# Performance work log

Hardware: AMD Instinct MI355X
Metric: run time of the kernel (lower is better)

Reference implementation:

```python
import jax, jax.numpy as jnp
import numpy as np

N_VOX = 200_000
C = 64
B, G = 2, 128  # batch size, grid resolution per axis
K = 27         # 3x3x3 kernel volume
EPS = 1e-5


def _build_coords_and_kernel_map(seed=0):
    """Build unique voxel coords on a [B,G,G,G] grid and the 27-offset kernel map.

    nbr[i, k] = row index of the voxel at coord[i] + offset[k], or N_VOX if absent
    (sentinel row that gathers zeros). This mirrors MinkowskiEngine's
    coordinate-hash in/out kernel maps for a stride-1 conv.
    """
    rng = np.random.default_rng(seed)
    total = B * G * G * G
    keys = np.sort(rng.choice(total, size=N_VOX, replace=False).astype(np.int64))
    z = keys % G
    y = (keys // G) % G
    x = (keys // (G * G)) % G
    b = keys // (G * G * G)
    offs = [(dx, dy, dz) for dx in (-1, 0, 1) for dy in (-1, 0, 1) for dz in (-1, 0, 1)]
    nbr = np.full((N_VOX, K), N_VOX, dtype=np.int64)
    for k, (dx, dy, dz) in enumerate(offs):
        nx, ny, nz = x + dx, y + dy, z + dz
        valid = (nx >= 0) & (nx < G) & (ny >= 0) & (ny < G) & (nz >= 0) & (nz < G)
        nkey = ((b * G + nx) * G + ny) * G + nz
        pos = np.clip(np.searchsorted(keys, nkey), 0, N_VOX - 1)
        found = valid & (keys[pos] == nkey)
        nbr[:, k] = np.where(found, pos, N_VOX)
    return jnp.asarray(nbr)


def setup_inputs() -> dict:
    key = jax.random.key(0)
    ks = jax.random.split(key, 12)
    w_scale = 1.0 / np.sqrt(K * C)
    inp = {
        "feats": jax.random.normal(ks[0], (N_VOX, C), jnp.float32),
        "nbr": _build_coords_and_kernel_map(),
        "W1": jax.random.normal(ks[1], (K, C, C), jnp.float32) * w_scale,
        "g1": 1.0 + 0.1 * jax.random.normal(ks[2], (C,), jnp.float32),
        "b1": 0.1 * jax.random.normal(ks[3], (C,), jnp.float32),
        "m1": 0.1 * jax.random.normal(ks[4], (C,), jnp.float32),
        "v1": jax.random.uniform(ks[5], (C,), jnp.float32, 0.5, 1.5),
        "W2": jax.random.normal(ks[6], (K, C, C), jnp.float32) * w_scale,
        "g2": 1.0 + 0.1 * jax.random.normal(ks[7], (C,), jnp.float32),
        "b2": 0.1 * jax.random.normal(ks[8], (C,), jnp.float32),
        "m2": 0.1 * jax.random.normal(ks[9], (C,), jnp.float32),
        "v2": jax.random.uniform(ks[10], (C,), jnp.float32, 0.5, 1.5),
    }
    return inp


def _bn(x, g, b, m, v):
    # MinkowskiBatchNorm, eval mode: per-channel affine with running stats
    return (x - m) * (g * jax.lax.rsqrt(v + EPS)) + b


def _sparse_conv(feats, nbr, W):
    # gather-GEMM-scatter sparse 3D conv over the precomputed kernel map.
    # Sentinel index N_VOX gathers the appended zero row (missing neighbor).
    fpad = jnp.concatenate([feats, jnp.zeros((1, feats.shape[1]), feats.dtype)], axis=0)
    out = jnp.zeros((feats.shape[0], W.shape[2]), feats.dtype)
    for k in range(W.shape[0]):  # fixed 27-tap loop (structural, not data dim)
        out = out + fpad[nbr[:, k]] @ W[k]
    return out


def reference(feats, nbr, W1, g1, b1, m1, v1, W2, g2, b2, m2, v2):
    h = jax.nn.relu(_bn(_sparse_conv(feats, nbr, W1), g1, b1, m1, v1))
    h = _bn(_sparse_conv(h, nbr, W2), g2, b2, m2, v2)
    # in_channels == out_channels and stride == 1 -> identity shortcut
    return jax.nn.relu(h + feats)
```

## Files before the change

### kernel.cpp

```cpp
#include <hip/hip_runtime.h>
#include <hip/hip_bf16.h>

#define NVOX 200000
#define NTAP 27
#define OSTR 68
#define ROWB 128

typedef __bf16          bf16x8 __attribute__((ext_vector_type(8)));
typedef unsigned short  u16x8  __attribute__((ext_vector_type(8)));
typedef float           f32x4  __attribute__((ext_vector_type(4)));

#define FB_BYTES    ((size_t)(NVOX + 1) * ROWB)
#define WSHUF_BYTES (NTAP * 2 * 4 * 64 * 16)
#define FB_OFF      0
#define H_OFF       (FB_BYTES)
#define WS1_OFF     (2 * FB_BYTES)
#define WS2_OFF     (WS1_OFF + WSHUF_BYTES)
#define FLAG_OFF    (WS2_OFF + WSHUF_BYTES)

static __device__ __forceinline__ unsigned short f2bf_bits(float f) {
    __hip_bfloat16 h = __float2bfloat16(f);
    union { __hip_bfloat16 h; unsigned short u; } u; u.h = h; return u.u;
}
static __device__ __forceinline__ float bf2f(unsigned short s) {
    union { float f; unsigned u; } u; u.u = ((unsigned)s) << 16; return u.f;
}
static __device__ __forceinline__ float ld_param(const void* p, int c, int isbf) {
    return isbf ? bf2f(((const unsigned short*)p)[c]) : ((const float*)p)[c];
}
static __device__ __forceinline__ void gload_lds16(const void* gp, void* lp) {
    __builtin_amdgcn_global_load_lds(
        (const __attribute__((address_space(1))) void*)gp,
        (__attribute__((address_space(3))) void*)lp, 16, 0, 0);
}
static __device__ __forceinline__ int wave_isbf(const unsigned* v1w) {
    int l = threadIdx.x & 63;
    int ok = 1;
    if (l < 32) {
        unsigned w = v1w[l], lo = w & 0xFFFFu, hi = w >> 16;
        ok = (lo >= 0x3F00u && lo <= 0x3FC0u && hi >= 0x3F00u && hi <= 0x3FC0u);
    }
    return __all(ok);
}

__global__ __launch_bounds__(256)
void prep_kernel(const void* __restrict__ feats,
                 const void* __restrict__ W1, const void* __restrict__ W2,
                 const unsigned* __restrict__ v1w, const unsigned* __restrict__ nbrw,
                 uint4* __restrict__ fbuf, uint4* __restrict__ hbuf,
                 uint4* __restrict__ Ws1, uint4* __restrict__ Ws2,
                 int* __restrict__ flags) {
    const int bx = blockIdx.x;
    if (bx < 6250) {
        const int isbf = wave_isbf(v1w);
        size_t t = (size_t)bx * 256 + threadIdx.x;
        if (isbf) {
            fbuf[t] = ((const uint4*)feats)[t];
        } else {
            float4 a = ((const float4*)feats)[2 * t];
            float4 b = ((const float4*)feats)[2 * t + 1];
            union { uint4 q; unsigned short u[8]; } o;
            o.u[0] = f2bf_bits(a.x); o.u[1] = f2bf_bits(a.y);
            o.u[2] = f2bf_bits(a.z); o.u[3] = f2bf_bits(a.w);
            o.u[4] = f2bf_bits(b.x); o.u[5] = f2bf_bits(b.y);
            o.u[6] = f2bf_bits(b.z); o.u[7] = f2bf_bits(b.w);
            fbuf[t] = o.q;
        }
    } else if (bx < 6358) {
        const int isbf = wave_isbf(v1w);
        int t = (bx - 6250) * 256 + threadIdx.x;
        const void* W = (t < 13824) ? W1 : W2;
        uint4* Ws     = (t < 13824) ? Ws1 : Ws2;
        int f = (t < 13824) ? t : t - 13824;
        int k  = f / 512;
        int r  = f % 512;
        int kc = r / 256;
        int r2 = r % 256;
        int nc = r2 / 64;
        int l  = r2 % 64;
        int quad = l >> 4, li = l & 15;
        unsigned short tmp[8];
#pragma unroll
        for (int j = 0; j < 8; ++j) {
            int off = k * 4096 + (kc * 32 + quad * 8 + j) * 64 + (nc * 16 + li);
            tmp[j] = isbf ? ((const unsigned short*)W)[off]
                          : f2bf_bits(((const float*)W)[off]);
        }
        uint4 v;
        v.x = (unsigned)tmp[0] | ((unsigned)tmp[1] << 16);
        v.y = (unsigned)tmp[2] | ((unsigned)tmp[3] << 16);
        v.z = (unsigned)tmp[4] | ((unsigned)tmp[5] << 16);
        v.w = (unsigned)tmp[6] | ((unsigned)tmp[7] << 16);
        Ws[f] = v;
    } else {
        int t = threadIdx.x;
        if (t < 64) {
            int isbf = wave_isbf(v1w);
            int n64ok = 1;
#pragma unroll
            for (int i = 0; i < 8; ++i)
                if (nbrw[2 * (t * 8 + i) + 1] != 0u) n64ok = 0;
            int n64 = __all(n64ok);
            if (t == 0) { flags[0] = isbf; flags[1] = n64; }
        }
        uint4 z = make_uint4(0u, 0u, 0u, 0u);
        if (t >= 64 && t < 72) fbuf[(size_t)NVOX * 8 + (t - 64)] = z;
        if (t >= 72 && t < 80) hbuf[(size_t)NVOX * 8 + (t - 72)] = z;
    }
}

#define STG(kk, bp) do {                                                    \
    if ((mgw >> (kk)) & 1) {                                                \
        int ia_ = nbrLDS[r0 * NTAP + (kk)];                                 \
        int ib_ = nbrLDS[r1 * NTAP + (kk)];                                 \
        gload_lds16(srcB + (size_t)ia_ * ROWB + f0 * 16,                    \
                    (void*)((bp) + w * 128));                               \
        gload_lds16(srcB + (size_t)ib_ * ROWB + f1 * 16,                    \
                    (void*)((bp) + w * 128 + 64));                         \
    } } while (0)

#define LOADB(kk, B0, B1) do {                                              \
    B0 = Ws[(kk) * 512 + w * 64 + l];                                       \
    B1 = Ws[(kk) * 512 + 256 + w * 64 + l];                                 \
} while (0)

#define COMPUTE(kk, bp, B0, B1) do {                                        \
    _Pragma("unroll")                                                       \
    for (int g = 0; g < 4; ++g) {                                           \
        if ((mg[g] >> (kk)) & 1) {                                          \
            bf16x8 a0_ = *(const bf16x8*)((bp) + ro0[g]);                   \
            bf16x8 a1_ = *(const bf16x8*)((bp) + ro1[g]);                   \
            acc[g] = __builtin_amdgcn_mfma_f32_16x16x32_bf16(a0_, B0, acc[g], 0, 0, 0); \
            acc[g] = __builtin_amdgcn_mfma_f32_16x16x32_bf16(a1_, B1, acc[g], 0, 0, 0); \
        }                                                                   \
    }                                                                       \
} while (0)

__global__ __launch_bounds__(256, 7)
void conv_bn_kernel(const uint4* __restrict__ srcV,
                    const void* __restrict__ nbr,
                    const bf16x8* __restrict__ Ws,
                    const void* __restrict__ gg, const void* __restrict__ bb,
                    const void* __restrict__ mm, const void* __restrict__ vv,
                    const u16x8* __restrict__ resid,
                    const int* __restrict__ flags,
                    void* __restrict__ dst, int final_out) {
    __shared__ __align__(16) int smi[5828];
    int*   nbrLDS = smi;
    uint4* at0    = (uint4*)(smi + 1728);
    uint4* at1    = at0 + 512;
    int*   maskLDS = smi + 5824;
    float* outLDS = (float*)smi;

    const int tid  = threadIdx.x;
    const int base = blockIdx.x * 64;
    const int isbf = flags[0];
    const int n64  = flags[1];
    const char* srcB = (const char*)srcV;

    if (tid < 4) maskLDS[tid] = 0;
    __syncthreads();
    {
        if (!n64) {
            const int* np = (const int*)nbr + (long)base * NTAP;
            for (int i = tid; i < 64 * NTAP; i += 256) nbrLDS[i] = np[i];
        } else {
            const long long* np = (const long long*)nbr + (long)base * NTAP;
            for (int i = tid; i < 64 * NTAP; i += 256) nbrLDS[i] = (int)np[i];
        }
    }
    __syncthreads();

    if (tid < NTAP * 4) {
        int k = tid >> 2, g = tid & 3;
        int mn = 0x7fffffff;
#pragma unroll
        for (int r = 0; r < 16; ++r) mn = min(mn, nbrLDS[(g * 16 + r) * NTAP + k]);
        if (mn < NVOX) atomicOr(&maskLDS[g], 1 << k);
    }
    __syncthreads();

    const int w = tid >> 6, l = tid & 63;
    const int quad = l >> 4, li = l & 15;

    int mg[4];
#pragma unroll
    for (int g = 0; g < 4; ++g) mg[g] = __builtin_amdgcn_readfirstlane(maskLDS[g]);
    const int mgw = __builtin_amdgcn_readfirstlane(maskLDS[w]);

    const int s0 = w * 128 + l;
    const int s1 = s0 + 64;
    const int r0 = s0 >> 3, f0 = (s0 - r0) & 7;
    const int r1 = s1 >> 3, f1 = (s1 - r1) & 7;
    int ro0[4], ro1[4];
#pragma unroll
    for (int g = 0; g < 4; ++g) {
        int row = g * 16 + li;
        ro0[g] = row * 8 + ((quad + row) & 7);
        ro1[g] = row * 8 + ((quad + 4 + row) & 7);
    }

    f32x4 acc[4];
#pragma unroll
    for (int g = 0; g < 4; ++g) acc[g] = (f32x4){0.f, 0.f, 0.f, 0.f};

    bf16x8 xB0, xB1, yB0, yB1;

    STG(0, at0);
    LOADB(0, xB0, xB1);
    __syncthreads();

    for (int k = 0; k < 26; k += 2) {
        STG(k + 1, at1);
        LOADB(k + 1, yB0, yB1);
        COMPUTE(k, at0, xB0, xB1);
        __syncthreads();
        STG(k + 2, at0);
        LOADB(k + 2, xB0, xB1);
        COMPUTE(k + 1, at1, yB0, yB1);
        __syncthreads();
    }
    COMPUTE(26, at0, xB0, xB1);

    const int c = w * 16 + li;
    float scale = ld_param(gg, c, isbf) * rsqrtf(ld_param(vv, c, isbf) + 1e-5f);
    float offs  = ld_param(bb, c, isbf) - ld_param(mm, c, isbf) * scale;

    __syncthreads();
#pragma unroll
    for (int g = 0; g < 4; ++g)
#pragma unroll
        for (int r = 0; r < 4; ++r)
            outLDS[(g * 16 + quad * 4 + r) * OSTR + c] = acc[g][r] * scale + offs;
    __syncthreads();

    {
        int trow = tid >> 2, cc = tid & 3;
        long grow = base + trow;
        const float4* lp = (const float4*)&outLDS[trow * OSTR + cc * 16];
        float4 q0 = lp[0], q1 = lp[1], q2 = lp[2], q3 = lp[3];
        float vals[16] = {q0.x, q0.y, q0.z, q0.w, q1.x, q1.y, q1.z, q1.w,
                          q2.x, q2.y, q2.z, q2.w, q3.x, q3.y, q3.z, q3.w};

        if (resid) {
            const u16x8* rp = resid + grow * 8 + cc * 2;
            u16x8 r0v = rp[0], r1v = rp[1];
#pragma unroll
            for (int j = 0; j < 8; ++j) { vals[j] += bf2f(r0v[j]); vals[8 + j] += bf2f(r1v[j]); }
        }
#pragma unroll
        for (int j = 0; j < 16; ++j) vals[j] = fmaxf(vals[j], 0.f);

        const int store_bf = (!final_out) || isbf;
        if (store_bf) {
            u16x8 o0, o1;
#pragma unroll
            for (int j = 0; j < 8; ++j) { o0[j] = f2bf_bits(vals[j]); o1[j] = f2bf_bits(vals[8 + j]); }
            u16x8* dp = (u16x8*)dst + grow * 8 + cc * 2;
            dp[0] = o0; dp[1] = o1;
        } else {
            float4* dp = (float4*)dst + grow * 16 + cc * 4;
            dp[0] = (float4){vals[0], vals[1], vals[2], vals[3]};
            dp[1] = (float4){vals[4], vals[5], vals[6], vals[7]};
            dp[2] = (float4){vals[8], vals[9], vals[10], vals[11]};
            dp[3] = (float4){vals[12], vals[13], vals[14], vals[15]};
        }
    }
}

extern "C" void kernel_launch(void* const* d_in, const int* in_sizes, int n_in,
                              void* d_out, int out_size, void* d_ws, size_t ws_size,
                              hipStream_t stream) {
    const void* feats = d_in[0];
    const void* nbr   = d_in[1];
    const void* W1    = d_in[2];
    const void* g1    = d_in[3];
    const void* b1    = d_in[4];
    const void* m1    = d_in[5];
    const void* v1    = d_in[6];
    const void* W2    = d_in[7];
    const void* g2    = d_in[8];
    const void* b2    = d_in[9];
    const void* m2    = d_in[10];
    const void* v2    = d_in[11];

    char* ws = (char*)d_ws;
    uint4* fbuf = (uint4*)(ws + FB_OFF);
    uint4* hbuf = (uint4*)(ws + H_OFF);
    uint4* Ws1  = (uint4*)(ws + WS1_OFF);
    uint4* Ws2  = (uint4*)(ws + WS2_OFF);
    int*   flags = (int*)(ws + FLAG_OFF);

    prep_kernel<<<dim3(6359), dim3(256), 0, stream>>>(
        feats, W1, W2, (const unsigned*)v1, (const unsigned*)nbr,
        fbuf, hbuf, Ws1, Ws2, flags);

    conv_bn_kernel<<<dim3(NVOX / 64), dim3(256), 0, stream>>>(
        fbuf, nbr, (const bf16x8*)Ws1, g1, b1, m1, v1,
        nullptr, flags, hbuf, 0);

    conv_bn_kernel<<<dim3(NVOX / 64), dim3(256), 0, stream>>>(
        hbuf, nbr, (const bf16x8*)Ws2, g2, b2, m2, v2,
        (const u16x8*)fbuf, flags, d_out, 1);
}
```

Baseline: 242.7 us.

## Stage two taps per pipeline step and remap blocks across XCDs

The gather/MFMA loop now stages two kernel taps per buffer, so each __syncthreads covers two taps, which halves the number of barriers and deepens the prefetch. Block indices are remapped so that consecutive voxel tiles land on the same XCD, which should improve L2 locality for neighbour gathers. Launch bounds drop from 7 to 4 waves per SIMD to make room for the larger LDS footprint and the extra B registers. The cost is lower occupancy and therefore less latency hiding.

```diff
diff --git a/kernel.cpp b/kernel.cpp
--- a/kernel.cpp
+++ b/kernel.cpp
@@ -119,9 +119,9 @@
                     (void*)((bp) + w * 128 + 64));                         \
     } } while (0)
 
-#define LOADB(kk, B0, B1) do {                                              \
-    B0 = Ws[(kk) * 512 + w * 64 + l];                                       \
-    B1 = Ws[(kk) * 512 + 256 + w * 64 + l];                                 \
+#define LOADB(kk, B0r, B1r) do {                                            \
+    B0r = Ws[(kk) * 512 + w * 64 + l];                                      \
+    B1r = Ws[(kk) * 512 + 256 + w * 64 + l];                                \
 } while (0)
 
 #define COMPUTE(kk, bp, B0, B1) do {                                        \
@@ -136,7 +136,7 @@
     }                                                                       \
 } while (0)
 
-__global__ __launch_bounds__(256, 7)
+__global__ __launch_bounds__(256, 4)
 void conv_bn_kernel(const uint4* __restrict__ srcV,
                     const void* __restrict__ nbr,
                     const bf16x8* __restrict__ Ws,
@@ -145,15 +145,23 @@
                     const u16x8* __restrict__ resid,
                     const int* __restrict__ flags,
                     void* __restrict__ dst, int final_out) {
-    __shared__ __align__(16) int smi[5828];
-    int*   nbrLDS = smi;
-    uint4* at0    = (uint4*)(smi + 1728);
-    uint4* at1    = at0 + 512;
-    int*   maskLDS = smi + 5824;
-    float* outLDS = (float*)smi;
+    __shared__ __align__(16) int smi[1732 + 4 * 2048];
+    int*   nbrLDS  = smi;
+    int*   maskLDS = smi + 1728;
+    uint4* at0     = (uint4*)(smi + 1732);
+    uint4* at0b    = at0 + 512;
+    uint4* at1     = at0 + 1024;
+    uint4* at1b    = at0 + 1536;
+    float* outLDS  = (float*)smi;
 
     const int tid  = threadIdx.x;
-    const int base = blockIdx.x * 64;
+    const int nwg  = gridDim.x;
+    const int orig = blockIdx.x;
+    const int qq   = nwg >> 3, rr = nwg & 7;
+    const int xcd  = orig & 7, idx = orig >> 3;
+    const int bid  = (xcd < rr ? xcd * (qq + 1) : rr * (qq + 1) + (xcd - rr) * qq) + idx;
+    const int base = bid * 64;
+
     const int isbf = flags[0];
     const int n64  = flags[1];
     const char* srcB = (const char*)srcV;
@@ -204,23 +212,30 @@
 #pragma unroll
     for (int g = 0; g < 4; ++g) acc[g] = (f32x4){0.f, 0.f, 0.f, 0.f};
 
-    bf16x8 xB0, xB1, yB0, yB1;
-
-    STG(0, at0);
-    LOADB(0, xB0, xB1);
-    __syncthreads();
-
-    for (int k = 0; k < 26; k += 2) {
-        STG(k + 1, at1);
-        LOADB(k + 1, yB0, yB1);
-        COMPUTE(k, at0, xB0, xB1);
+    bf16x8 xB0, xB1, xB2, xB3, yB0, yB1, yB2, yB3;
+
+    STG(0, at0); STG(1, at0b);
+    LOADB(0, xB0, xB1); LOADB(1, xB2, xB3);
+    __syncthreads();
+
+    for (int k = 0; k < 24; k += 4) {
+        STG(k + 2, at1); STG(k + 3, at1b);
+        LOADB(k + 2, yB0, yB1); LOADB(k + 3, yB2, yB3);
+        COMPUTE(k,     at0,  xB0, xB1);
+        COMPUTE(k + 1, at0b, xB2, xB3);
         __syncthreads();
-        STG(k + 2, at0);
-        LOADB(k + 2, xB0, xB1);
-        COMPUTE(k + 1, at1, yB0, yB1);
+        STG(k + 4, at0); STG(k + 5, at0b);
+        LOADB(k + 4, xB0, xB1); LOADB(k + 5, xB2, xB3);
+        COMPUTE(k + 2, at1,  yB0, yB1);
+        COMPUTE(k + 3, at1b, yB2, yB3);
         __syncthreads();
     }
-    COMPUTE(26, at0, xB0, xB1);
+    STG(26, at1);
+    LOADB(26, yB0, yB1);
+    COMPUTE(24, at0,  xB0, xB1);
+    COMPUTE(25, at0b, xB2, xB3);
+    __syncthreads();
+    COMPUTE(26, at1, yB0, yB1);
 
     const int c = w * 16 + li;
     float scale = ld_param(gg, c, isbf) * rsqrtf(ld_param(vv, c, isbf) + 1e-5f);
```

Result: slower. 272.3 us (+12.2%).

## Shrink conv tiles to 32 voxels with 2-wave blocks and XCD-aware block remap

Applied to the files above, without the earlier changes.

Each conv block now handles 32 voxels with 128 threads instead of 64 voxels with 256 threads. Each wave computes two 16-channel output groups, so it holds four weight fragments per tap and issues four MFMAs per row group. Block indices are remapped so consecutive voxel chunks land on the same XCD, which should improve L2 locality of neighbor gathers. The smaller tiles give more blocks, less LDS per block and finer tap masks. In exchange, weight fragments are reloaded twice as often per voxel and each wave needs more registers.

```diff
diff --git a/kernel.cpp b/kernel.cpp
--- a/kernel.cpp
+++ b/kernel.cpp
@@ -5,6 +5,7 @@
 #define NTAP 27
 #define OSTR 68
 #define ROWB 128
+#define VPB  32
 
 typedef __bf16          bf16x8 __attribute__((ext_vector_type(8)));
 typedef unsigned short  u16x8  __attribute__((ext_vector_type(8)));
@@ -119,24 +120,28 @@
                     (void*)((bp) + w * 128 + 64));                         \
     } } while (0)
 
-#define LOADB(kk, B0, B1) do {                                              \
-    B0 = Ws[(kk) * 512 + w * 64 + l];                                       \
-    B1 = Ws[(kk) * 512 + 256 + w * 64 + l];                                 \
+#define LOADB4(kk, B00r, B01r, B10r, B11r) do {                             \
+    B00r = Ws[(kk) * 512 +       (2 * w) * 64 + l];                         \
+    B01r = Ws[(kk) * 512 + 256 + (2 * w) * 64 + l];                         \
+    B10r = Ws[(kk) * 512 +       (2 * w + 1) * 64 + l];                     \
+    B11r = Ws[(kk) * 512 + 256 + (2 * w + 1) * 64 + l];                     \
 } while (0)
 
-#define COMPUTE(kk, bp, B0, B1) do {                                        \
+#define COMPUTE(kk, bp, B00, B01, B10, B11) do {                            \
     _Pragma("unroll")                                                       \
-    for (int g = 0; g < 4; ++g) {                                           \
+    for (int g = 0; g < 2; ++g) {                                           \
         if ((mg[g] >> (kk)) & 1) {                                          \
             bf16x8 a0_ = *(const bf16x8*)((bp) + ro0[g]);                   \
             bf16x8 a1_ = *(const bf16x8*)((bp) + ro1[g]);                   \
-            acc[g] = __builtin_amdgcn_mfma_f32_16x16x32_bf16(a0_, B0, acc[g], 0, 0, 0); \
-            acc[g] = __builtin_amdgcn_mfma_f32_16x16x32_bf16(a1_, B1, acc[g], 0, 0, 0); \
+            acc[2*g+0] = __builtin_amdgcn_mfma_f32_16x16x32_bf16(a0_, B00, acc[2*g+0], 0, 0, 0); \
+            acc[2*g+0] = __builtin_amdgcn_mfma_f32_16x16x32_bf16(a1_, B01, acc[2*g+0], 0, 0, 0); \
+            acc[2*g+1] = __builtin_amdgcn_mfma_f32_16x16x32_bf16(a0_, B10, acc[2*g+1], 0, 0, 0); \
+            acc[2*g+1] = __builtin_amdgcn_mfma_f32_16x16x32_bf16(a1_, B11, acc[2*g+1], 0, 0, 0); \
         }                                                                   \
     }                                                                       \
 } while (0)
 
-__global__ __launch_bounds__(256, 7)
+__global__ __launch_bounds__(128, 6)
 void conv_bn_kernel(const uint4* __restrict__ srcV,
                     const void* __restrict__ nbr,
                     const bf16x8* __restrict__ Ws,
@@ -145,34 +150,40 @@
                     const u16x8* __restrict__ resid,
                     const int* __restrict__ flags,
                     void* __restrict__ dst, int final_out) {
-    __shared__ __align__(16) int smi[5828];
-    int*   nbrLDS = smi;
-    uint4* at0    = (uint4*)(smi + 1728);
-    uint4* at1    = at0 + 512;
-    int*   maskLDS = smi + 5824;
-    float* outLDS = (float*)smi;
+    __shared__ __align__(16) int smi[868 + 2 * 1024];
+    int*   nbrLDS  = smi;
+    int*   maskLDS = smi + 864;
+    uint4* at0     = (uint4*)(smi + 868);
+    uint4* at1     = at0 + 256;
+    float* outLDS  = (float*)smi;
 
     const int tid  = threadIdx.x;
-    const int base = blockIdx.x * 64;
+    const int nwg  = gridDim.x;
+    const int orig = blockIdx.x;
+    const int qq   = nwg >> 3, rr = nwg & 7;
+    const int xcd  = orig & 7, idx = orig >> 3;
+    const int bid  = (xcd < rr ? xcd * (qq + 1) : rr * (qq + 1) + (xcd - rr) * qq) + idx;
+    const int base = bid * VPB;
+
     const int isbf = flags[0];
     const int n64  = flags[1];
     const char* srcB = (const char*)srcV;
 
-    if (tid < 4) maskLDS[tid] = 0;
+    if (tid < 2) maskLDS[tid] = 0;
     __syncthreads();
     {
         if (!n64) {
             const int* np = (const int*)nbr + (long)base * NTAP;
-            for (int i = tid; i < 64 * NTAP; i += 256) nbrLDS[i] = np[i];
+            for (int i = tid; i < VPB * NTAP; i += 128) nbrLDS[i] = np[i];
         } else {
             const long long* np = (const long long*)nbr + (long)base * NTAP;
-            for (int i = tid; i < 64 * NTAP; i += 256) nbrLDS[i] = (int)np[i];
-        }
-    }
-    __syncthreads();
-
-    if (tid < NTAP * 4) {
-        int k = tid >> 2, g = tid & 3;
+            for (int i = tid; i < VPB * NTAP; i += 128) nbrLDS[i] = (int)np[i];
+        }
+    }
+    __syncthreads();
+
+    if (tid < NTAP * 2) {
+        int k = tid >> 1, g = tid & 1;
         int mn = 0x7fffffff;
 #pragma unroll
         for (int r = 0; r < 16; ++r) mn = min(mn, nbrLDS[(g * 16 + r) * NTAP + k]);
@@ -183,18 +194,18 @@
     const int w = tid >> 6, l = tid & 63;
     const int quad = l >> 4, li = l & 15;
 
-    int mg[4];
-#pragma unroll
-    for (int g = 0; g < 4; ++g) mg[g] = __builtin_amdgcn_readfirstlane(maskLDS[g]);
-    const int mgw = __builtin_amdgcn_readfirstlane(maskLDS[w]);
+    int mg[2];
+#pragma unroll
+    for (int g = 0; g < 2; ++g) mg[g] = __builtin_amdgcn_readfirstlane(maskLDS[g]);
+    const int mgw = mg[0] | mg[1] ? __builtin_amdgcn_readfirstlane(maskLDS[w]) : 0;
 
     const int s0 = w * 128 + l;
     const int s1 = s0 + 64;
     const int r0 = s0 >> 3, f0 = (s0 - r0) & 7;
     const int r1 = s1 >> 3, f1 = (s1 - r1) & 7;
-    int ro0[4], ro1[4];
-#pragma unroll
-    for (int g = 0; g < 4; ++g) {
+    int ro0[2], ro1[2];
+#pragma unroll
+    for (int g = 0; g < 2; ++g) {
         int row = g * 16 + li;
         ro0[g] = row * 8 + ((quad + row) & 7);
         ro1[g] = row * 8 + ((quad + 4 + row) & 7);
@@ -204,34 +215,39 @@
 #pragma unroll
     for (int g = 0; g < 4; ++g) acc[g] = (f32x4){0.f, 0.f, 0.f, 0.f};
 
-    bf16x8 xB0, xB1, yB0, yB1;
+    bf16x8 xB00, xB01, xB10, xB11, yB00, yB01, yB10, yB11;
 
     STG(0, at0);
-    LOADB(0, xB0, xB1);
+    LOADB4(0, xB00, xB01, xB10, xB11);
     __syncthreads();
 
     for (int k = 0; k < 26; k += 2) {
         STG(k + 1, at1);
-        LOADB(k + 1, yB0, yB1);
-        COMPUTE(k, at0, xB0, xB1);
+        LOADB4(k + 1, yB00, yB01, yB10, yB11);
+        COMPUTE(k, at0, xB00, xB01, xB10, xB11);
         __syncthreads();
         STG(k + 2, at0);
-        LOADB(k + 2, xB0, xB1);
-        COMPUTE(k + 1, at1, yB0, yB1);
+        LOADB4(k + 2, xB00, xB01, xB10, xB11);
+        COMPUTE(k + 1, at1, yB00, yB01, yB10, yB11);
         __syncthreads();
     }
-    COMPUTE(26, at0, xB0, xB1);
-
-    const int c = w * 16 + li;
-    float scale = ld_param(gg, c, isbf) * rsqrtf(ld_param(vv, c, isbf) + 1e-5f);
-    float offs  = ld_param(bb, c, isbf) - ld_param(mm, c, isbf) * scale;
-
-    __syncthreads();
-#pragma unroll
-    for (int g = 0; g < 4; ++g)
-#pragma unroll
-        for (int r = 0; r < 4; ++r)
-            outLDS[(g * 16 + quad * 4 + r) * OSTR + c] = acc[g][r] * scale + offs;
+    COMPUTE(26, at0, xB00, xB01, xB10, xB11);
+
+    const int c0 = w * 32 + li;
+    const int c1 = c0 + 16;
+    float sc0 = ld_param(gg, c0, isbf) * rsqrtf(ld_param(vv, c0, isbf) + 1e-5f);
+    float of0 = ld_param(bb, c0, isbf) - ld_param(mm, c0, isbf) * sc0;
+    float sc1 = ld_param(gg, c1, isbf) * rsqrtf(ld_param(vv, c1, isbf) + 1e-5f);
+    float of1 = ld_param(bb, c1, isbf) - ld_param(mm, c1, isbf) * sc1;
+
+    __syncthreads();
+#pragma unroll
+    for (int g = 0; g < 2; ++g)
+#pragma unroll
+        for (int r = 0; r < 4; ++r) {
+            outLDS[(g * 16 + quad * 4 + r) * OSTR + c0] = acc[2*g+0][r] * sc0 + of0;
+            outLDS[(g * 16 + quad * 4 + r) * OSTR + c1] = acc[2*g+1][r] * sc1 + of1;
+        }
     __syncthreads();
 
     {
@@ -295,11 +311,11 @@
         feats, W1, W2, (const unsigned*)v1, (const unsigned*)nbr,
         fbuf, hbuf, Ws1, Ws2, flags);
 
-    conv_bn_kernel<<<dim3(NVOX / 64), dim3(256), 0, stream>>>(
+    conv_bn_kernel<<<dim3(NVOX / VPB), dim3(128), 0, stream>>>(
         fbuf, nbr, (const bf16x8*)Ws1, g1, b1, m1, v1,
         nullptr, flags, hbuf, 0);
 
-    conv_bn_kernel<<<dim3(NVOX / 64), dim3(256), 0, stream>>>(
+    conv_bn_kernel<<<dim3(NVOX / VPB), dim3(128), 0, stream>>>(
         hbuf, nbr, (const bf16x8*)Ws2, g2, b2, m2, v2,
         (const u16x8*)fbuf, flags, d_out, 1);
 }
```

Measured after the change: 626.1 us. +157.9%, slower.
